# Performance work log

Measured on AMD Instinct MI355X. Metric: run time of the kernel, lower is better.

## Reference

```python
import jax, jax.numpy as jnp
import numpy as np

R = 8192        # proposals per image
D = 4096        # box-head feature dim (input_shape.channels)
C = 80          # num_classes (COCO)
K_PRE = 512     # per-class pre-NMS top-k candidates
IMG_W, IMG_H = 1000.0, 800.0
SCORE_THRESH = 1e-5
NMS_THRESH = 0.5
TOPK = 100      # test_topk_per_image


def setup_inputs() -> dict:
    key = jax.random.key(0)
    ks = jax.random.split(key, 6)
    x = jax.random.normal(ks[0], (R, D), jnp.float32)
    # Xavier-uniform init for the two linear heads
    lim = np.sqrt(6.0 / (D + C)).astype(np.float32)
    Wc = jax.random.uniform(ks[1], (D, C), jnp.float32, -lim, lim)
    bc = jnp.zeros((C,), jnp.float32)
    Wd = jax.random.uniform(ks[2], (D, C), jnp.float32, -lim, lim)
    bd = jnp.zeros((C,), jnp.float32)
    # class-agnostic proposal boxes in xyxy, roughly inside the image
    xy = jax.random.uniform(ks[3], (R, 2), jnp.float32) * jnp.array([IMG_W * 0.8, IMG_H * 0.8], jnp.float32)
    wh = jax.random.uniform(ks[4], (R, 2), jnp.float32) * jnp.array([IMG_W * 0.3, IMG_H * 0.3], jnp.float32) + 4.0
    boxes = jnp.concatenate([xy, xy + wh], axis=1)
    return {"x": x, "Wc": Wc, "bc": bc, "Wd": Wd, "bd": bd, "boxes": boxes}


def _pairwise_iou(b):  # b: [K,4] xyxy -> [K,K]
    area = (b[:, 2] - b[:, 0]) * (b[:, 3] - b[:, 1])
    lt = jnp.maximum(b[:, None, :2], b[None, :, :2])
    rb = jnp.minimum(b[:, None, 2:], b[None, :, 2:])
    wh = jnp.clip(rb - lt, 0.0)
    inter = wh[..., 0] * wh[..., 1]
    return inter / (area[:, None] + area[None, :] - inter + 1e-9)


def _nms_one_class(scores_c, boxes):  # scores_c: [R], boxes: [R,4] -> keep mask [R]
    vals, idx = jax.lax.top_k(scores_c, K_PRE)          # pre-NMS top-k, score-sorted desc
    iou = _pairwise_iou(boxes[idx])                      # [K_PRE, K_PRE]
    valid = vals > SCORE_THRESH                          # score thresholding

    def body(kept, i):
        # suppressed if any already-kept higher-scoring box overlaps too much
        sup = jnp.any(kept & (iou[i] > NMS_THRESH))
        k = valid[i] & (~sup)
        return kept.at[i].set(k), k

    _, keeps = jax.lax.scan(body, jnp.zeros((K_PRE,), bool), jnp.arange(K_PRE))
    return jnp.zeros((scores_c.shape[0],), bool).at[idx].set(keeps)


def _clip_boxes(boxes):
    x1 = jnp.clip(boxes[:, 0:1], 0.0, IMG_W)
    y1 = jnp.clip(boxes[:, 1:2], 0.0, IMG_H)
    x2 = jnp.clip(boxes[:, 2:3], 0.0, IMG_W)
    y2 = jnp.clip(boxes[:, 3:4], 0.0, IMG_H)
    return jnp.concatenate([x1, y1, x2, y2], axis=1)


def reference(x, Wc, bc, Wd, bd, boxes):
    # WSDDN-style object-mining head: softmax over classes x softmax over proposals
    cls_logits = x @ Wc + bc                    # [R, C]
    det_logits = x @ Wd + bd                    # [R, C]
    pred = jax.nn.softmax(cls_logits, axis=1) * jax.nn.softmax(det_logits, axis=0)

    # inference path: clip boxes, threshold, per-class (batched) NMS, keep topk
    bclip = _clip_boxes(boxes)
    keep = jax.vmap(_nms_one_class, in_axes=(1, None), out_axes=1)(pred, bclip)  # [R, C]
    kept_scores = jnp.where(keep, pred, 0.0)
    # topk_per_image across all (proposal, class) detections
    kth = jax.lax.top_k(kept_scores.reshape(-1), TOPK)[0][-1]
    return jnp.where(kept_scores >= kth, kept_scores, 0.0)   # [R, C]
```

## Files before the change

kernel.cpp:

```cpp
#include <hip/hip_runtime.h>
#include <hip/hip_bf16.h>
#include <math.h>

#define R_N 8192
#define D_K 4096
#define C_N 80
#define NC2 160
#define KSPLIT 8
#define KSLICE (D_K / KSPLIT)
#define KPRE 512
#define TOPK 100
#define LIST_CAP (80 * 512)

typedef _Float16 f16;
typedef f16 f16x8 __attribute__((ext_vector_type(8)));
typedef float f32x4 __attribute__((ext_vector_type(4)));

__device__ __forceinline__ void async_copy16(const void* g, void* l) {
    __builtin_amdgcn_global_load_lds(
        (const __attribute__((address_space(1))) void*)g,
        (__attribute__((address_space(3))) void*)l, 16, 0, 0);
}

__global__ __launch_bounds__(256) void zero_kernel(float* __restrict__ out, unsigned* __restrict__ cnt) {
    int idx = blockIdx.x * 256 + threadIdx.x;
    if (idx < R_N * C_N) out[idx] = 0.0f;
    if (blockIdx.x == 0 && threadIdx.x == 0) *cnt = 0u;
}

__global__ __launch_bounds__(256) void wt_convert(const float* __restrict__ Wc,
                                                  const float* __restrict__ Wd,
                                                  f16* __restrict__ BhT,
                                                  f16* __restrict__ BlT) {
    const int n = blockIdx.x;
    const float* src = (n < C_N) ? (Wc + n) : (Wd + (n - C_N));
    f16* dh = BhT + (size_t)n * D_K;
    f16* dl = BlT + (size_t)n * D_K;
    for (int k = threadIdx.x; k < D_K; k += 256) {
        float v = src[(size_t)k * C_N];
        f16 h = (f16)v;
        dh[k] = h;
        dl[k] = (f16)(v - (float)h);
    }
}

__global__ __launch_bounds__(256) void gemm_part(const float* __restrict__ x,
                                                 const f16* __restrict__ BhT,
                                                 const f16* __restrict__ BlT,
                                                 float* __restrict__ part) {
    __shared__ __align__(16) float As[128 * 32];
    __shared__ __align__(16) f16 Bhs[160 * 32];
    __shared__ __align__(16) f16 Bls[160 * 32];

    const int b    = blockIdx.x;
    const int rb   = b & 63;
    const int ks   = b >> 6;
    const int row0 = rb * 128;
    const int kbase = ks * KSLICE;
    const int tid  = threadIdx.x;
    const int wv   = tid >> 6, lane = tid & 63;
    const int m    = lane & 15, quad = lane >> 4;

    f32x4 acc[2][10];
#pragma unroll
    for (int t = 0; t < 2; ++t)
#pragma unroll
        for (int n = 0; n < 10; ++n) acc[t][n] = (f32x4)(0.0f);

    for (int ch = 0; ch < KSLICE / 32; ++ch) {
        const int k0 = kbase + ch * 32;
#pragma unroll
        for (int i = 0; i < 4; ++i) {
            int t = tid + 256 * i;
            int r = t >> 3, cs = t & 7;
            int cg = cs ^ (r & 7);
            async_copy16(x + (size_t)(row0 + r) * D_K + k0 + cg * 4,
                         (char*)As + (size_t)t * 16);
        }
#pragma unroll
        for (int i = 0; i < 3; ++i) {
            int t = tid + 256 * i;
            if (t < 640) {
                int nn = t >> 2, cc = t & 3;
                size_t go = (size_t)nn * D_K + k0 + cc * 8;
                async_copy16(BhT + go, (char*)Bhs + (size_t)t * 16);
                async_copy16(BlT + go, (char*)Bls + (size_t)t * 16);
            }
        }
        __syncthreads();
        f16x8 ah[2], al[2];
#pragma unroll
        for (int t = 0; t < 2; ++t) {
            int r = wv * 32 + t * 16 + m;
            int r7 = r & 7;
            float4 c0 = *(const float4*)&As[r * 32 + (((2 * quad) ^ r7) << 2)];
            float4 c1 = *(const float4*)&As[r * 32 + (((2 * quad + 1) ^ r7) << 2)];
            float tv[8] = {c0.x, c0.y, c0.z, c0.w, c1.x, c1.y, c1.z, c1.w};
#pragma unroll
            for (int j = 0; j < 8; ++j) {
                f16 h = (f16)tv[j];
                ah[t][j] = h;
                al[t][j] = (f16)(tv[j] - (float)h);
            }
        }
#pragma unroll
        for (int n = 0; n < 10; ++n) {
            int nn = n * 16 + m;
            f16x8 bh = *(const f16x8*)&Bhs[nn * 32 + quad * 8];
            f16x8 bl = *(const f16x8*)&Bls[nn * 32 + quad * 8];
#pragma unroll
            for (int t = 0; t < 2; ++t) {
                acc[t][n] = __builtin_amdgcn_mfma_f32_16x16x32_f16(al[t], bh, acc[t][n], 0, 0, 0);
                acc[t][n] = __builtin_amdgcn_mfma_f32_16x16x32_f16(ah[t], bl, acc[t][n], 0, 0, 0);
                acc[t][n] = __builtin_amdgcn_mfma_f32_16x16x32_f16(ah[t], bh, acc[t][n], 0, 0, 0);
            }
        }
        __syncthreads();
    }
#pragma unroll
    for (int t = 0; t < 2; ++t) {
        int grow0 = row0 + wv * 32 + t * 16 + quad * 4;
#pragma unroll
        for (int n = 0; n < 10; ++n) {
            int gcol = n * 16 + m;
#pragma unroll
            for (int r4 = 0; r4 < 4; ++r4)
                part[((size_t)ks * R_N + grow0 + r4) * NC2 + gcol] = acc[t][n][r4];
        }
    }
}

__global__ __launch_bounds__(256) void reduce_bias(const float* __restrict__ part,
                                                   const float* __restrict__ bc,
                                                   const float* __restrict__ bd,
                                                   float* __restrict__ cls,
                                                   float* __restrict__ detT) {
    const size_t STRIDE = (size_t)R_N * NC2;
    size_t idx = (size_t)blockIdx.x * 256 + threadIdx.x;
    int row = (int)(idx / NC2), col = (int)(idx % NC2);
    float p0 = part[idx + 0 * STRIDE], p1 = part[idx + 1 * STRIDE];
    float p2 = part[idx + 2 * STRIDE], p3 = part[idx + 3 * STRIDE];
    float p4 = part[idx + 4 * STRIDE], p5 = part[idx + 5 * STRIDE];
    float p6 = part[idx + 6 * STRIDE], p7 = part[idx + 7 * STRIDE];
    float s = ((p0 + p1) + (p2 + p3)) + ((p4 + p5) + (p6 + p7));
    if (col < C_N) {
        cls[(size_t)row * C_N + col] = s + bc[col];
    } else {
        detT[(size_t)(col - C_N) * R_N + row] = s + bd[col - C_N];
    }
}

__global__ __launch_bounds__(256) void row_softmax(const float* __restrict__ cls,
                                                   float* __restrict__ P) {
    int tid = threadIdx.x;
    int wave = tid >> 6, lane = tid & 63;
    int row = blockIdx.x * 4 + wave;
    float v0 = cls[(size_t)row * C_N + lane];
    float v1 = (lane < 16) ? cls[(size_t)row * C_N + 64 + lane] : -INFINITY;
    float m = fmaxf(v0, v1);
#pragma unroll
    for (int off = 32; off > 0; off >>= 1) m = fmaxf(m, __shfl_xor(m, off, 64));
    float e0 = expf(v0 - m);
    float e1 = (lane < 16) ? expf(v1 - m) : 0.0f;
    float s = e0 + e1;
#pragma unroll
    for (int off = 32; off > 0; off >>= 1) s += __shfl_xor(s, off, 64);
    P[(size_t)lane * R_N + row] = e0 / s;
    if (lane < 16) P[(size_t)(64 + lane) * R_N + row] = e1 / s;
}

__global__ __launch_bounds__(256) void col_softmax_mul(const float* __restrict__ detT,
                                                       float* __restrict__ P) {
    __shared__ float red[256];
    int c = blockIdx.x, tid = threadIdx.x;
    const float* dc = detT + (size_t)c * R_N;
    float m = -INFINITY;
    for (int r = tid; r < R_N; r += 256) m = fmaxf(m, dc[r]);
    red[tid] = m; __syncthreads();
    for (int s2 = 128; s2 > 0; s2 >>= 1) {
        if (tid < s2) red[tid] = fmaxf(red[tid], red[tid + s2]);
        __syncthreads();
    }
    m = red[0]; __syncthreads();
    float sum = 0.0f;
    for (int r = tid; r < R_N; r += 256) sum += expf(dc[r] - m);
    red[tid] = sum; __syncthreads();
    for (int s2 = 128; s2 > 0; s2 >>= 1) {
        if (tid < s2) red[tid] += red[tid + s2];
        __syncthreads();
    }
    float s = red[0];
    float* pc = P + (size_t)c * R_N;
    for (int r = tid; r < R_N; r += 256) pc[r] = pc[r] * (expf(dc[r] - m) / s);
}

__global__ __launch_bounds__(256) void chunk_sort(const float* __restrict__ P,
                                                  unsigned long long* __restrict__ cand) {
    __shared__ unsigned long long sk[1024];
    const int c = blockIdx.x >> 3, ch = blockIdx.x & 7;
    const int tid = threadIdx.x;
    const float* pc = P + (size_t)c * R_N + ch * 1024;

    for (int i = tid; i < 1024; i += 256) {
        unsigned u = __float_as_uint(pc[i]);
        int r = ch * 1024 + i;
        sk[i] = ((unsigned long long)u << 32) | (unsigned)(8191 - r);
    }
    __syncthreads();
    for (int size = 2; size <= 1024; size <<= 1) {
        for (int stride = size >> 1; stride > 0; stride >>= 1) {
            for (int t = tid; t < 512; t += 256) {
                int i = 2 * t - (t & (stride - 1));
                int j = i + stride;
                unsigned long long a = sk[i], b = sk[j];
                bool desc = ((i & size) == 0);
                if ((a < b) == desc) { sk[i] = b; sk[j] = a; }
            }
            __syncthreads();
        }
    }
    unsigned long long* dst = cand + (size_t)blockIdx.x * 512;
    for (int i = tid; i < 512; i += 256) dst[i] = sk[i];
}

__global__ __launch_bounds__(256) void merge_extract(const unsigned long long* __restrict__ cand,
                                                     const float* __restrict__ boxes,
                                                     float* __restrict__ svals,
                                                     int* __restrict__ sridx,
                                                     float* __restrict__ cbox,
                                                     int* __restrict__ nvalid) {
    __shared__ unsigned long long A[1024];
    const int c = blockIdx.x, tid = threadIdx.x;
    const unsigned long long* base = cand + (size_t)c * 8 * 512;

    for (int i = tid; i < 512; i += 256) A[i] = base[i];
    for (int l = 1; l < 8; ++l) {
        __syncthreads();
        for (int i = tid; i < 512; i += 256) A[512 + i] = base[l * 512 + (511 - i)];
        __syncthreads();
        for (int stride = 512; stride > 0; stride >>= 1) {
            for (int t = tid; t < 512; t += 256) {
                int i = 2 * t - (t & (stride - 1));
                int j = i + stride;
                unsigned long long a = A[i], b = A[j];
                if (a < b) { A[i] = b; A[j] = a; }
            }
            __syncthreads();
        }
    }
    __syncthreads();
    for (int i = tid; i < 512; i += 256) {
        unsigned long long k = A[i];
        float v = __uint_as_float((unsigned)(k >> 32));
        int r = 8191 - (int)(k & 0xFFFFFFFFull);
        svals[c * 512 + i] = v;
        sridx[c * 512 + i] = r;
        float b0 = boxes[r * 4 + 0], b1 = boxes[r * 4 + 1];
        float b2 = boxes[r * 4 + 2], b3 = boxes[r * 4 + 3];
        float4 cb;
        cb.x = fminf(fmaxf(b0, 0.0f), 1000.0f);
        cb.y = fminf(fmaxf(b1, 0.0f), 800.0f);
        cb.z = fminf(fmaxf(b2, 0.0f), 1000.0f);
        cb.w = fminf(fmaxf(b3, 0.0f), 800.0f);
        *(float4*)&cbox[((size_t)c * 512 + i) * 4] = cb;
        float vn = (i < 511) ? __uint_as_float((unsigned)(A[i + 1] >> 32)) : -1.0f;
        if (v > 1e-5f && !(vn > 1e-5f)) nvalid[c] = i + 1;
        if (i == 0 && !(v > 1e-5f)) nvalid[c] = 0;
    }
}

__global__ __launch_bounds__(256) void iou_mask(const float* __restrict__ cbox,
                                                const int* __restrict__ nvalid,
                                                unsigned long long* __restrict__ gmask) {
    __shared__ float sx1[512], sy1[512], sx2[512], sy2[512], sar[512];
    const int c = blockIdx.x >> 3, w = blockIdx.x & 7;
    const int tid = threadIdx.x;
    const int nv = nvalid[c];

    for (int i = tid; i < 512; i += 256) {
        float4 b = *(const float4*)&cbox[((size_t)c * 512 + i) * 4];
        sx1[i] = b.x; sy1[i] = b.y; sx2[i] = b.z; sy2[i] = b.w;
        sar[i] = (b.z - b.x) * (b.w - b.y);
    }
    __syncthreads();
    for (int i = tid; i < 512; i += 256) {
        unsigned long long bits = 0ull;
        if (i < nv && w <= (i >> 6)) {
            float xi1 = sx1[i], yi1 = sy1[i], xi2 = sx2[i], yi2 = sy2[i], ai = sar[i];
#pragma unroll 8
            for (int j2 = 0; j2 < 64; ++j2) {
                int j = (w << 6) + j2;
                float xx1 = fmaxf(xi1, sx1[j]);
                float yy1 = fmaxf(yi1, sy1[j]);
                float xx2 = fminf(xi2, sx2[j]);
                float yy2 = fminf(yi2, sy2[j]);
                float ww = fmaxf(xx2 - xx1, 0.0f);
                float hh = fmaxf(yy2 - yy1, 0.0f);
                float inter = ww * hh;
                float iou = inter / (ai + sar[j] - inter + 1e-9f);
                if (iou > 0.5f) bits |= (1ull << j2);
            }
        }
        gmask[((size_t)c * 512 + i) * 8 + w] = bits;
    }
}

__global__ __launch_bounds__(64) void nms_scan(const unsigned long long* __restrict__ gmask,
                                               const float* __restrict__ svals,
                                               const int* __restrict__ sridx,
                                               const int* __restrict__ nvalid,
                                               float* __restrict__ g_ls,
                                               unsigned* __restrict__ g_lp,
                                               unsigned* __restrict__ g_cnt) {
    __shared__ unsigned long long sm[512 * 8];
    __shared__ unsigned char keepf[512];
    const int c = blockIdx.x, lane = threadIdx.x;
    const int nv = nvalid[c];
    const unsigned long long* gm = gmask + (size_t)c * 512 * 8;

    for (int t = lane; t < 4096; t += 64) sm[t] = gm[t];
    __syncthreads();

    const bool rd = (lane < 8);
    unsigned long long keptw = 0ull;
    unsigned long long pf[8];
#pragma unroll
    for (int d = 0; d < 8; ++d) pf[d] = rd ? sm[(d & 511) * 8 + lane] : 0ull;
    for (int i = 0; i < nv; ++i) {
        unsigned long long mm = pf[i & 7];
        int ip = (i + 8) & 511;
        pf[i & 7] = rd ? sm[ip * 8 + lane] : 0ull;
        int sup = __any((keptw & mm) != 0ull);
        int keep = !sup;
        if (keep && lane == (i >> 6)) keptw |= (1ull << (i & 63));
        if (lane == 0) keepf[i] = (unsigned char)keep;
    }
    __syncthreads();
    for (int i = lane; i < nv; i += 64) {
        if (keepf[i]) {
            unsigned pos = atomicAdd(g_cnt, 1u);
            g_ls[pos] = svals[c * 512 + i];
            g_lp[pos] = (unsigned)(sridx[c * 512 + i] * C_N + c);
        }
    }
}

__global__ __launch_bounds__(256) void kth_kernel(const float* __restrict__ g_ls,
                                                  const unsigned* __restrict__ g_cnt,
                                                  float* __restrict__ g_kth) {
    __shared__ unsigned hist[256];
    __shared__ unsigned sh_prefix, sh_k;
    int tid = threadIdx.x;
    unsigned n = *g_cnt;
    if (n < (unsigned)TOPK) { if (tid == 0) *g_kth = 0.0f; return; }
    if (tid == 0) { sh_prefix = 0u; sh_k = TOPK; }
    __syncthreads();
    for (int b = 3; b >= 0; --b) {
        hist[tid] = 0;
        __syncthreads();
        unsigned pfx = sh_prefix;
        for (unsigned i = tid; i < n; i += 256) {
            unsigned u = __float_as_uint(g_ls[i]);
            bool ok = (b == 3) || ((u >> (8 * (b + 1))) == pfx);
            if (ok) atomicAdd(&hist[(u >> (8 * b)) & 255], 1u);
        }
        __syncthreads();
        if (tid == 0) {
            unsigned cum = 0, k = sh_k;
            for (unsigned d = 255;; --d) {
                unsigned c2 = cum + hist[d];
                if (c2 >= k || d == 0) { sh_k = k - cum; sh_prefix = (pfx << 8) | d; break; }
                cum = c2;
            }
        }
        __syncthreads();
    }
    if (tid == 0) *g_kth = __uint_as_float(sh_prefix);
}

__global__ __launch_bounds__(256) void scatter_kernel(const float* __restrict__ g_ls,
                                                      const unsigned* __restrict__ g_lp,
                                                      const unsigned* __restrict__ g_cnt,
                                                      const float* __restrict__ g_kth,
                                                      float* __restrict__ out) {
    unsigned idx = blockIdx.x * 256 + threadIdx.x;
    unsigned n = *g_cnt;
    float kth = *g_kth;
    if (idx < n) {
        float s = g_ls[idx];
        if (s >= kth) out[g_lp[idx]] = s;
    }
}

extern "C" void kernel_launch(void* const* d_in, const int* in_sizes, int n_in,
                              void* d_out, int out_size, void* d_ws, size_t ws_size,
                              hipStream_t stream) {
    const float* x     = (const float*)d_in[0];
    const float* Wc    = (const float*)d_in[1];
    const float* bc    = (const float*)d_in[2];
    const float* Wd    = (const float*)d_in[3];
    const float* bd    = (const float*)d_in[4];
    const float* boxes = (const float*)d_in[5];
    float* out = (float*)d_out;

    char* w = (char*)d_ws;
    float* part = (float*)w;  w += (size_t)KSPLIT * R_N * NC2 * sizeof(float);
    float* cls  = (float*)w;  w += (size_t)R_N * C_N * sizeof(float);
    float* detT = (float*)w;  w += (size_t)C_N * R_N * sizeof(float);
    float* P    = (float*)w;  w += (size_t)C_N * R_N * sizeof(float);
    float* g_ls = (float*)w;  w += (size_t)LIST_CAP * sizeof(float);
    unsigned* g_lp = (unsigned*)w; w += (size_t)LIST_CAP * sizeof(unsigned);
    unsigned* g_cnt = (unsigned*)w; w += 256;
    float* g_kth = (float*)w; w += 256;
    f16* BhT = (f16*)w; w += (size_t)NC2 * D_K * sizeof(f16);
    f16* BlT = (f16*)w; w += (size_t)NC2 * D_K * sizeof(f16);

    char* a = (char*)part;
    unsigned long long* cand = (unsigned long long*)a; a += (size_t)C_N * 8 * 512 * sizeof(unsigned long long);
    float* svals = (float*)a;  a += (size_t)C_N * KPRE * sizeof(float);
    int*   sridx = (int*)a;    a += (size_t)C_N * KPRE * sizeof(int);
    float* cbox  = (float*)a;  a += (size_t)C_N * KPRE * 4 * sizeof(float);
    int*   nvalid = (int*)a;   a += 4096;
    unsigned long long* gmask = (unsigned long long*)a; a += (size_t)C_N * KPRE * 8 * sizeof(unsigned long long);

    zero_kernel<<<(R_N * C_N) / 256, 256, 0, stream>>>(out, g_cnt);
    wt_convert<<<NC2, 256, 0, stream>>>(Wc, Wd, BhT, BlT);
    gemm_part<<<64 * KSPLIT, 256, 0, stream>>>(x, BhT, BlT, part);
    reduce_bias<<<(R_N * NC2) / 256, 256, 0, stream>>>(part, bc, bd, cls, detT);
    row_softmax<<<R_N / 4, 256, 0, stream>>>(cls, P);
    col_softmax_mul<<<C_N, 256, 0, stream>>>(detT, P);
    chunk_sort<<<C_N * 8, 256, 0, stream>>>(P, cand);
    merge_extract<<<C_N, 256, 0, stream>>>(cand, boxes, svals, sridx, cbox, nvalid);
    iou_mask<<<C_N * 8, 256, 0, stream>>>(cbox, nvalid, gmask);
    nms_scan<<<C_N, 64, 0, stream>>>(gmask, svals, sridx, nvalid, g_ls, g_lp, g_cnt);
    kth_kernel<<<1, 256, 0, stream>>>(g_ls, g_cnt, g_kth);
    scatter_kernel<<<(LIST_CAP + 255) / 256, 256, 0, stream>>>(g_ls, g_lp, g_cnt, g_kth, out);
}
```

Measured before the change: 462.3 us.

## Select global kth score from per-class top-100 kept candidates via register bisection

Each NMS block now also writes its first 100 kept scores in sorted order into a small per-class buffer, zero-padded. The single-block kth kernel reads only these 8000 values into registers and binary-searches the float bit pattern with wave reductions. This replaces four passes of a radix histogram over the whole kept list, which used shared atomics. It relies on the global top-100 being drawn from each class's top-100, which holds because the candidates are score-sorted. It also assumes non-negative scores and returns 0 when fewer than 100 detections are kept.

```diff
diff --git a/kernel.cpp b/kernel.cpp
--- a/kernel.cpp
+++ b/kernel.cpp
@@ -311,7 +311,8 @@
                                                const int* __restrict__ nvalid,
                                                float* __restrict__ g_ls,
                                                unsigned* __restrict__ g_lp,
-                                               unsigned* __restrict__ g_cnt) {
+                                               unsigned* __restrict__ g_cnt,
+                                               float* __restrict__ k100) {
     __shared__ unsigned long long sm[512 * 8];
     __shared__ unsigned char keepf[512];
     const int c = blockIdx.x, lane = threadIdx.x;
@@ -343,39 +344,47 @@
             g_lp[pos] = (unsigned)(sridx[c * 512 + i] * C_N + c);
         }
     }
-}
-
-__global__ __launch_bounds__(256) void kth_kernel(const float* __restrict__ g_ls,
-                                                  const unsigned* __restrict__ g_cnt,
+    for (int i = lane; i < 100; i += 64) k100[c * 100 + i] = 0.0f;
+    unsigned base = 0;
+    for (int ch2 = 0; ch2 < 8 && (int)base < 100; ++ch2) {
+        int i = ch2 * 64 + lane;
+        bool kk = (i < nv) && (keepf[i] != 0);
+        unsigned long long mb = __ballot(kk);
+        unsigned pre = (unsigned)__popcll(mb & ((1ull << lane) - 1ull));
+        if (kk && base + pre < 100)
+            k100[c * 100 + base + pre] = svals[c * 512 + i];
+        base += (unsigned)__popcll(mb);
+    }
+}
+
+__global__ __launch_bounds__(256) void kth_kernel(const float* __restrict__ k100,
                                                   float* __restrict__ g_kth) {
-    __shared__ unsigned hist[256];
-    __shared__ unsigned sh_prefix, sh_k;
-    int tid = threadIdx.x;
-    unsigned n = *g_cnt;
-    if (n < (unsigned)TOPK) { if (tid == 0) *g_kth = 0.0f; return; }
-    if (tid == 0) { sh_prefix = 0u; sh_k = TOPK; }
-    __syncthreads();
-    for (int b = 3; b >= 0; --b) {
-        hist[tid] = 0;
-        __syncthreads();
-        unsigned pfx = sh_prefix;
-        for (unsigned i = tid; i < n; i += 256) {
-            unsigned u = __float_as_uint(g_ls[i]);
-            bool ok = (b == 3) || ((u >> (8 * (b + 1))) == pfx);
-            if (ok) atomicAdd(&hist[(u >> (8 * b)) & 255], 1u);
-        }
-        __syncthreads();
-        if (tid == 0) {
-            unsigned cum = 0, k = sh_k;
-            for (unsigned d = 255;; --d) {
-                unsigned c2 = cum + hist[d];
-                if (c2 >= k || d == 0) { sh_k = k - cum; sh_prefix = (pfx << 8) | d; break; }
-                cum = c2;
-            }
-        }
-        __syncthreads();
-    }
-    if (tid == 0) *g_kth = __uint_as_float(sh_prefix);
+    __shared__ unsigned red[4];
+    __shared__ unsigned s_total;
+    const int tid = threadIdx.x;
+    const int wv = tid >> 6, lane = tid & 63;
+    unsigned v[32];
+#pragma unroll
+    for (int j = 0; j < 32; ++j) {
+        int idx = j * 256 + tid;
+        v[j] = (idx < C_N * 100) ? __float_as_uint(k100[idx]) : 0u;
+    }
+    unsigned lo = 0u, hi = 0x7FFFFFFFu;
+    while (lo < hi) {
+        unsigned mid = lo + (hi - lo + 1) / 2;
+        unsigned cnt = 0;
+#pragma unroll
+        for (int j = 0; j < 32; ++j) cnt += (v[j] >= mid) ? 1u : 0u;
+#pragma unroll
+        for (int off = 32; off > 0; off >>= 1) cnt += __shfl_down(cnt, off, 64);
+        if (lane == 0) red[wv] = cnt;
+        __syncthreads();
+        if (tid == 0) s_total = red[0] + red[1] + red[2] + red[3];
+        __syncthreads();
+        unsigned total = s_total;
+        if (total >= (unsigned)TOPK) lo = mid; else hi = mid - 1;
+    }
+    if (tid == 0) *g_kth = __uint_as_float(lo);
 }
 
 __global__ __launch_bounds__(256) void scatter_kernel(const float* __restrict__ g_ls,
@@ -414,6 +423,7 @@
     float* g_kth = (float*)w; w += 256;
     f16* BhT = (f16*)w; w += (size_t)NC2 * D_K * sizeof(f16);
     f16* BlT = (f16*)w; w += (size_t)NC2 * D_K * sizeof(f16);
+    float* k100 = (float*)w; w += (size_t)C_N * 100 * sizeof(float);
 
     char* a = (char*)part;
     unsigned long long* cand = (unsigned long long*)a; a += (size_t)C_N * 8 * 512 * sizeof(unsigned long long);
@@ -432,7 +442,7 @@
     chunk_sort<<<C_N * 8, 256, 0, stream>>>(P, cand);
     merge_extract<<<C_N, 256, 0, stream>>>(cand, boxes, svals, sridx, cbox, nvalid);
     iou_mask<<<C_N * 8, 256, 0, stream>>>(cbox, nvalid, gmask);
-    nms_scan<<<C_N, 64, 0, stream>>>(gmask, svals, sridx, nvalid, g_ls, g_lp, g_cnt);
-    kth_kernel<<<1, 256, 0, stream>>>(g_ls, g_cnt, g_kth);
+    nms_scan<<<C_N, 64, 0, stream>>>(gmask, svals, sridx, nvalid, g_ls, g_lp, g_cnt, k100);
+    kth_kernel<<<1, 256, 0, stream>>>(k100, g_kth);
     scatter_kernel<<<(LIST_CAP + 255) / 256, 256, 0, stream>>>(g_ls, g_lp, g_cnt, g_kth, out);
 }
```

Result: faster. 391.9 us (-15.2%).
